# Performance work log

Hardware: AMD Instinct MI355X
Metric: run time of the kernel (lower is better)

## Reference

```python
import jax, jax.numpy as jnp
import numpy as np

N = 50000          # nodes
E = 400000         # edges
MUL0 = 16          # multiplicity of 0e irreps (node & message)
MUL1 = 8           # multiplicity of 1o irreps
RBF = 8
HID = 64
CUTOFF = 5.0
WNUM = MUL0*MUL0 + MUL1*MUL0 + MUL0*MUL1 + MUL1*MUL1  # 576 tp weights per edge
EPS = 1e-8
INV_SQRT3 = 1.0 / np.sqrt(3.0).astype(np.float32)
A_PATH = 1.0 / np.sqrt(float(MUL0 + MUL1))  # e3nn path normalization (fan_in = 24 for both outputs)


def _split_sv(x):
    # x: [n, 40] -> scalars [n,16], vectors [n,8,3]
    return x[:, :MUL0], x[:, MUL0:].reshape(-1, MUL1, 3)


def _irrep_norm(x):
    # RMS-normalize each irrep block separately (IrrepNorm)
    s, v = _split_sv(x)
    s_rms = jnp.sqrt(jnp.mean(s * s, axis=-1, keepdims=True) + EPS)
    v_rms = jnp.sqrt(jnp.mean(jnp.sum(v * v, axis=-1), axis=-1, keepdims=True) + EPS)
    return jnp.concatenate([s / s_rms, (v / v_rms[:, :, None]).reshape(-1, MUL1 * 3)], axis=-1)


def setup_inputs() -> dict:
    key = jax.random.key(0)
    ks = jax.random.split(key, 20)
    inp = {
        'x': jax.random.normal(ks[0], (N, MUL0 + 3 * MUL1), jnp.float32),
        'edge_src': jax.random.randint(ks[1], (E,), 0, N, jnp.int32),
        'edge_dst': jax.random.randint(ks[2], (E,), 0, N, jnp.int32),
        'edge_sh': jax.random.normal(ks[3], (E, 4), jnp.float32),
        'edge_rbf': jax.random.uniform(ks[4], (E, RBF), jnp.float32),
        'edge_len': jax.random.uniform(ks[5], (E,), jnp.float32) * CUTOFF,
        # radial MLP producing per-edge TP weights
        'w_r1': jax.random.normal(ks[6], (RBF, HID), jnp.float32) / np.sqrt(RBF),
        'b_r1': jnp.zeros((HID,), jnp.float32),
        'w_r2': jax.random.normal(ks[7], (HID, WNUM), jnp.float32) / np.sqrt(HID),
        'b_r2': jnp.zeros((WNUM,), jnp.float32),
        # edge gate MLP
        'w_g1': jax.random.normal(ks[8], (RBF, HID), jnp.float32) / np.sqrt(RBF),
        'b_g1': jnp.zeros((HID,), jnp.float32),
        'w_g2': jax.random.normal(ks[9], (HID, 1), jnp.float32) / np.sqrt(HID),
        'b_g2': jnp.zeros((1,), jnp.float32),
        # msg_linear: 16x0e+8x1o -> (16x0e scalars + 8x0e gates) + 8x1o gated
        'Wm_s': jax.random.normal(ks[10], (MUL0, MUL0 + MUL1), jnp.float32),
        'Wm_v': jax.random.normal(ks[11], (MUL1, MUL1), jnp.float32),
        # update_linear and self_linear: 16x0e+8x1o -> 16x0e+8x1o
        'Wu_s': jax.random.normal(ks[12], (MUL0, MUL0), jnp.float32),
        'Wu_v': jax.random.normal(ks[13], (MUL1, MUL1), jnp.float32),
        'Ws_s': jax.random.normal(ks[14], (MUL0, MUL0), jnp.float32),
        'Ws_v': jax.random.normal(ks[15], (MUL1, MUL1), jnp.float32),
        'res_scale': jnp.asarray(0.1, jnp.float32),
    }
    return inp


def reference(x, edge_src, edge_dst, edge_sh, edge_rbf, edge_len,
              w_r1, b_r1, w_r2, b_r2, w_g1, b_g1, w_g2, b_g2,
              Wm_s, Wm_v, Wu_s, Wu_v, Ws_s, Ws_v, res_scale):
    x_norm = _irrep_norm(x)
    xs, xv = _split_sv(x_norm)

    # per-edge TP weights from radial MLP
    w = jax.nn.silu(edge_rbf @ w_r1 + b_r1) @ w_r2 + b_r2            # [E, 576]
    o = MUL0 * MUL0
    w1 = w[:, :o].reshape(-1, MUL0, MUL0)                            # 0e x 0e -> 0e
    w2 = w[:, o:o + MUL1 * MUL0].reshape(-1, MUL1, MUL0)             # 1o x 1o -> 0e
    o += MUL1 * MUL0
    w3 = w[:, o:o + MUL0 * MUL1].reshape(-1, MUL0, MUL1)             # 0e x 1o -> 1o
    o += MUL0 * MUL1
    w4 = w[:, o:].reshape(-1, MUL1, MUL1)                            # 1o x 0e -> 1o

    # gather per-edge source features
    s_e = xs[edge_src]                                               # [E,16]
    v_e = xv[edge_src]                                               # [E,8,3]
    sh0 = edge_sh[:, :1]                                             # [E,1]
    sh1 = edge_sh[:, 1:4]                                            # [E,3]

    # fully-connected tensor product (CG for l<=1, component norm, path norm)
    m0 = A_PATH * (jnp.einsum('ei,eij->ej', s_e * sh0, w1)
                   + INV_SQRT3 * jnp.einsum('eic,ec,eij->ej', v_e, sh1, w2))   # [E,16]
    m1 = A_PATH * (jnp.einsum('ei,eij,ec->ejc', s_e, w3, sh1)
                   + jnp.einsum('eic,eij->ejc', v_e * sh0[:, :, None], w4))    # [E,8,3]

    # cutoff and sigmoid edge gate
    cw = 0.5 * (jnp.cos(jnp.pi * edge_len / CUTOFF) + 1.0) * (edge_len < CUTOFF)
    gw = jax.nn.sigmoid(jax.nn.silu(edge_rbf @ w_g1 + b_g1) @ w_g2 + b_g2)     # [E,1]
    ew = cw[:, None] * gw                                                      # [E,1]
    m0 = m0 * ew
    m1 = m1 * ew[:, :, None]

    # scatter-add into destination nodes, normalize by total edge weight
    agg0 = jax.ops.segment_sum(m0, edge_dst, num_segments=N)                   # [N,16]
    agg1 = jax.ops.segment_sum(m1.reshape(-1, MUL1 * 3), edge_dst, num_segments=N).reshape(-1, MUL1, 3)
    norm = jax.ops.segment_sum(ew, edge_dst, num_segments=N)                   # [N,1]
    norm = jnp.maximum(norm, EPS)
    agg0 = agg0 / norm
    agg1 = agg1 / norm[:, :, None]

    # msg_linear (equivariant linear, fan-in normalized)
    sc = agg0 @ Wm_s / np.sqrt(MUL0)                                           # [N,24]
    vv = jnp.einsum('nic,ij->njc', agg1, Wm_v) / np.sqrt(MUL1)                 # [N,8,3]

    # gated nonlinearity
    scal = jax.nn.silu(sc[:, :MUL0])
    gates = jax.nn.sigmoid(sc[:, MUL0:])
    vg = vv * gates[:, :, None]

    # update + self interaction, residual
    out_s = scal @ Wu_s / np.sqrt(MUL0) + xs @ Ws_s / np.sqrt(MUL0)
    out_v = (jnp.einsum('nic,ij->njc', vg, Wu_v) + jnp.einsum('nic,ij->njc', xv, Ws_v)) / np.sqrt(MUL1)
    out = jnp.concatenate([out_s, out_v.reshape(-1, MUL1 * 3)], axis=-1)
    return x + res_scale * out
```

## Files before the change

kernel.cpp:

```cpp
#include <hip/hip_runtime.h>
#include <cstdint>

#define MUL0 16
#define MUL1 8
#define NRBF 8
#define HID 64
#define WNUM 576
#define CUTOFF 5.0f
#define EPSF 1e-8f

#define INV_SQRT3 0.57735026918962576f
#define A_PATH    0.20412414523193154f
#define Q16       0.25f
#define Q8        0.35355339059327373f
#define PI_OVER_CUT 0.62831853071795865f

typedef _Float16 f16;
typedef _Float16 f16x8 __attribute__((ext_vector_type(8)));
typedef float f32x4 __attribute__((ext_vector_type(4)));

#define MFMA16(a, b, cc) __builtin_amdgcn_mfma_f32_16x16x32_f16(a, b, cc, 0, 0, 0)

__device__ __forceinline__ float sigm(float x) { return 1.0f / (1.0f + __expf(-x)); }

typedef __attribute__((address_space(1))) const unsigned char* gptr_t;
typedef __attribute__((address_space(3))) unsigned char* lptr_t;

__device__ __forceinline__ void stage16(const void* g, void* l) {
  __builtin_amdgcn_global_load_lds((gptr_t)g, (lptr_t)l, 16, 0, 0);
}

extern "C" __global__ __launch_bounds__(256) void k_pre(
    const float* __restrict__ x, float* __restrict__ xnorm,
    float* __restrict__ agg0, float* __restrict__ agg1,
    float* __restrict__ normb, const float* __restrict__ w_r2,
    f16* __restrict__ W2T, int N) {
  int gid = blockIdx.x * 256 + threadIdx.x;

  if (gid < HID * WNUM) {
    int n = gid >> 6, k = gid & 63;
    int jt = n >> 4, cc = n & 15;
    int h = k >> 3, e = k & 7;
    int dst = jt * 1024 + cc * 64 + ((h ^ (cc & 7)) << 3) + e;
    W2T[dst] = (f16)w_r2[k * WNUM + n];
  }

  if (gid < N) {
    long long n = gid;
    const float4* xr = (const float4*)(x + n * 40);
    float4 vv[10];
#pragma unroll
    for (int i = 0; i < 10; i++) vv[i] = xr[i];
    float* f = (float*)vv;
    float ss = 0.f, vs = 0.f;
#pragma unroll
    for (int i = 0; i < 16; i++) ss += f[i] * f[i];
#pragma unroll
    for (int i = 16; i < 40; i++) vs += f[i] * f[i];
    float sr = rsqrtf(ss * (1.0f / 16.0f) + EPSF);
    float vr = rsqrtf(vs * (1.0f / 8.0f) + EPSF);
#pragma unroll
    for (int i = 0; i < 16; i++) f[i] *= sr;
#pragma unroll
    for (int i = 16; i < 40; i++) f[i] *= vr;
    float4* o = (float4*)(xnorm + n * 40);
#pragma unroll
    for (int i = 0; i < 10; i++) o[i] = vv[i];
    float4 z = {0.f, 0.f, 0.f, 0.f};
    float4* pa0 = (float4*)(agg0 + n * 16);
#pragma unroll
    for (int i = 0; i < 4; i++) pa0[i] = z;
    float4* pa1 = (float4*)(agg1 + n * 24);
#pragma unroll
    for (int i = 0; i < 6; i++) pa1[i] = z;
    normb[n] = 0.f;
  }
}

extern "C" __global__ __launch_bounds__(256, 3) void k_edge(
    const float* __restrict__ xnorm,
    const int* __restrict__ esrc, const int* __restrict__ edst,
    const float* __restrict__ sh, const float* __restrict__ rbf,
    const float* __restrict__ elen,
    const float* __restrict__ w_r1, const float* __restrict__ b_r1,
    const float* __restrict__ w_g1, const float* __restrict__ b_g1,
    const float* __restrict__ w_g2, const float* __restrict__ b_g2,
    const float* __restrict__ b_r2, const f16* __restrict__ W2T,
    float* __restrict__ agg0, float* __restrict__ agg1,
    float* __restrict__ normb, int E) {
  __shared__ __align__(16) char smem[53248];
  f16   (*s_H)[32][72]  = (f16(*)[32][72])(smem);
  float (*s_sn)[32][20] = (float(*)[32][20])(smem + 18432);
  float (*s_v)[32][26]  = (float(*)[32][26])(smem + 28672);
  float (*s_a1)[32][10] = (float(*)[32][10])(smem + 41984);
  float (*s_sh)[32][4]  = (float(*)[32][4])(smem + 47104);
  float (*s_rbf)[32][8] = (float(*)[32][8])(smem + 49152);
  float* s_bias = (float*)(smem + 49152);

  const int t = threadIdx.x;
  const int w = t >> 6;
  const int lane = t & 63;
  const long long eb = (long long)blockIdx.x * 128 + w * 32;

  int dstv = 0, srcv = 0;
  float lenv = 1e9f;
  if (lane < 32) {
    long long g2 = eb + lane;
    float4 shv = {0.f, 0.f, 0.f, 0.f};
    if (g2 < E) {
      srcv = esrc[g2];
      dstv = edst[g2];
      lenv = elen[g2];
      shv = *(const float4*)&sh[g2 * 4];
    }
    *(float4*)&s_sh[w][lane][0] = shv;
  }
  {
    int e = lane >> 1, half = lane & 1;
    long long ge2 = eb + e;
    float4 rv4 = {0.f, 0.f, 0.f, 0.f};
    if (ge2 < E) rv4 = *(const float4*)&rbf[ge2 * 8 + half * 4];
    *(float4*)&s_rbf[w][e][half * 4] = rv4;
  }
  __syncthreads();

  {
    const int ge_l = lane >> 2;
    const int part = lane & 3;
#pragma unroll
    for (int g = 0; g < 2; g++) {
      int e = g * 16 + ge_l;
      int srcn = __shfl(srcv, e);
      const float* xr = xnorm + (long long)srcn * 40;
      if (part < 2) {
        float4 aLo = *(const float4*)(xr + part * 8);
        float4 aHi = *(const float4*)(xr + part * 8 + 4);
        *(float4*)&s_sn[w][e][part * 8] = aLo;
        *(float4*)&s_sn[w][e][part * 8 + 4] = aHi;
      } else {
        const int i0 = (part - 2) * 4;
        const float* vp = xr + 16 + i0 * 3;
        float4 v0 = *(const float4*)(vp);
        float4 v1 = *(const float4*)(vp + 4);
        float4 v2 = *(const float4*)(vp + 8);
        *(float4*)&s_v[w][e][i0 * 3] = v0;
        *(float4*)&s_v[w][e][i0 * 3 + 4] = v1;
        *(float4*)&s_v[w][e][i0 * 3 + 8] = v2;
        float4 shq = *(const float4*)&s_sh[w][e][0];
        float s1x = shq.y, s1y = shq.z, s1z = shq.w;
        s_a1[w][e][i0]     = INV_SQRT3 * (v0.x * s1x + v0.y * s1y + v0.z * s1z);
        s_a1[w][e][i0 + 1] = INV_SQRT3 * (v0.w * s1x + v1.x * s1y + v1.y * s1z);
        s_a1[w][e][i0 + 2] = INV_SQRT3 * (v1.z * s1x + v1.w * s1y + v2.x * s1z);
        s_a1[w][e][i0 + 3] = INV_SQRT3 * (v2.y * s1x + v2.z * s1y + v2.w * s1z);
      }
    }
  }

  {
    float wr[8];
#pragma unroll
    for (int r = 0; r < 8; r++) wr[r] = w_r1[r * HID + lane];
    float bh = b_r1[lane];
#pragma unroll 4
    for (int u = 0; u < 32; u++) {
      float4 ra = *(const float4*)&s_rbf[w][u][0];
      float4 rb2 = *(const float4*)&s_rbf[w][u][4];
      float acc = bh + ra.x * wr[0] + ra.y * wr[1] + ra.z * wr[2] + ra.w * wr[3]
                     + rb2.x * wr[4] + rb2.y * wr[5] + rb2.z * wr[6] + rb2.w * wr[7];
      s_H[w][u][lane] = (f16)(acc * sigm(acc));
    }
  }

  float ewv = 0.f;
  {
    const int eg = lane & 31;
    const int hf = lane >> 5;
    float4 ga = *(const float4*)&s_rbf[w][eg][0];
    float4 gb = *(const float4*)&s_rbf[w][eg][4];
    float rv[8] = {ga.x, ga.y, ga.z, ga.w, gb.x, gb.y, gb.z, gb.w};
    float accp = 0.f;
#pragma unroll
    for (int ch = 0; ch < 2; ch++) {
      const int base = hf * 32 + ch * 16;
      float ttv[16];
      {
        const float4 b0 = *(const float4*)&b_g1[base];
        const float4 b1 = *(const float4*)&b_g1[base + 4];
        const float4 b2 = *(const float4*)&b_g1[base + 8];
        const float4 b3 = *(const float4*)&b_g1[base + 12];
        ttv[0] = b0.x; ttv[1] = b0.y; ttv[2] = b0.z; ttv[3] = b0.w;
        ttv[4] = b1.x; ttv[5] = b1.y; ttv[6] = b1.z; ttv[7] = b1.w;
        ttv[8] = b2.x; ttv[9] = b2.y; ttv[10] = b2.z; ttv[11] = b2.w;
        ttv[12] = b3.x; ttv[13] = b3.y; ttv[14] = b3.z; ttv[15] = b3.w;
      }
#pragma unroll
      for (int r = 0; r < 8; r++) {
        const float* wg = w_g1 + r * HID + base;
        float4 w0 = *(const float4*)(wg);
        float4 w1 = *(const float4*)(wg + 4);
        float4 w2 = *(const float4*)(wg + 8);
        float4 w3 = *(const float4*)(wg + 12);
        float rr = rv[r];
        ttv[0] += rr * w0.x; ttv[1] += rr * w0.y; ttv[2] += rr * w0.z; ttv[3] += rr * w0.w;
        ttv[4] += rr * w1.x; ttv[5] += rr * w1.y; ttv[6] += rr * w1.z; ttv[7] += rr * w1.w;
        ttv[8] += rr * w2.x; ttv[9] += rr * w2.y; ttv[10] += rr * w2.z; ttv[11] += rr * w2.w;
        ttv[12] += rr * w3.x; ttv[13] += rr * w3.y; ttv[14] += rr * w3.z; ttv[15] += rr * w3.w;
      }
      const float4 g0 = *(const float4*)&w_g2[base];
      const float4 g1 = *(const float4*)&w_g2[base + 4];
      const float4 g2 = *(const float4*)&w_g2[base + 8];
      const float4 g3 = *(const float4*)&w_g2[base + 12];
      float gw[16] = {g0.x, g0.y, g0.z, g0.w, g1.x, g1.y, g1.z, g1.w,
                      g2.x, g2.y, g2.z, g2.w, g3.x, g3.y, g3.z, g3.w};
#pragma unroll
      for (int k = 0; k < 16; k++) accp += ttv[k] * sigm(ttv[k]) * gw[k];
    }
    accp += __shfl_xor(accp, 32);
    if (lane < 32) {
      long long g2e = eb + lane;
      if (g2e < E) {
        float cw = (lenv < CUTOFF) ? 0.5f * (__cosf(PI_OVER_CUT * lenv) + 1.0f) : 0.f;
        ewv = cw * sigm(accp + b_g2[0]);
      }
    }
  }
  __syncthreads();

  const int quad = lane >> 4;
  const int c = lane & 15;

  const f16x8 af00 = *(const f16x8*)&s_H[w][c][quad * 8];
  const f16x8 af01 = *(const f16x8*)&s_H[w][c][32 + quad * 8];
  const f16x8 af10 = *(const f16x8*)&s_H[w][16 + c][quad * 8];
  const f16x8 af11 = *(const f16x8*)&s_H[w][16 + c][32 + quad * 8];
  for (int i = t; i < WNUM; i += 256) s_bias[i] = b_r2[i];
  __syncthreads();

  char* ring = smem;
  const char* W2Tc = (const char*)W2T;
  const int lofs = w * 1024;
  const int gofs = w * 1024 + lane * 16;

  stage16(W2Tc + gofs, ring + lofs);
  stage16(W2Tc + 4096 + gofs, ring + 4096 + lofs);

  const int rd0 = c * 128 + ((quad ^ (c & 7)) << 4);
  const int rd1 = c * 128 + (((quad + 4) ^ (c & 7)) << 4);

  float p1[2][4] = {{0.f}}, p2[2][4] = {{0.f}}, t3[2][4] = {{0.f}};
  float mx[2][4] = {{0.f}}, my[2][4] = {{0.f}}, mz[2][4] = {{0.f}};

#pragma unroll 1
  for (int ch = 0; ch < 4; ch++) {
    __syncthreads();
    stage16(W2Tc + (ch + 1) * 8192 + gofs, ring + ((ch + 1) & 1) * 8192 + lofs);
    stage16(W2Tc + (ch + 1) * 8192 + 4096 + gofs,
            ring + ((ch + 1) & 1) * 8192 + 4096 + lofs);
    const char* bb = ring + (ch & 1) * 8192;
#pragma unroll
    for (int q = 0; q < 4; q++) {
      const int jt = ch * 4 + q;
      const char* tb = bb + q * 2048;
      f16x8 b0 = *(const f16x8*)(tb + rd0);
      f16x8 b1 = *(const f16x8*)(tb + rd1);
      float bias = s_bias[jt * 16 + c];
      f32x4 C0 = {0.f, 0.f, 0.f, 0.f};
      C0 = MFMA16(af00, b0, C0); C0 = MFMA16(af01, b1, C0);
      f32x4 C1 = {0.f, 0.f, 0.f, 0.f};
      C1 = MFMA16(af10, b0, C1); C1 = MFMA16(af11, b1, C1);
#pragma unroll
      for (int r = 0; r < 4; r++) {
        p1[0][r] += s_sn[w][quad * 4 + r][jt] * (C0[r] + bias);
        p1[1][r] += s_sn[w][16 + quad * 4 + r][jt] * (C1[r] + bias);
      }
    }
  }
#pragma unroll 1
  for (int ch = 4; ch < 6; ch++) {
    __syncthreads();
    stage16(W2Tc + (ch + 1) * 8192 + gofs, ring + ((ch + 1) & 1) * 8192 + lofs);
    stage16(W2Tc + (ch + 1) * 8192 + 4096 + gofs,
            ring + ((ch + 1) & 1) * 8192 + 4096 + lofs);
    const char* bb = ring + (ch & 1) * 8192;
#pragma unroll
    for (int q = 0; q < 4; q++) {
      const int jt = ch * 4 + q;
      const char* tb = bb + q * 2048;
      f16x8 b0 = *(const f16x8*)(tb + rd0);
      f16x8 b1 = *(const f16x8*)(tb + rd1);
      float bias = s_bias[jt * 16 + c];
      f32x4 C0 = {0.f, 0.f, 0.f, 0.f};
      C0 = MFMA16(af00, b0, C0); C0 = MFMA16(af01, b1, C0);
      f32x4 C1 = {0.f, 0.f, 0.f, 0.f};
      C1 = MFMA16(af10, b0, C1); C1 = MFMA16(af11, b1, C1);
      const int i = jt - 16;
#pragma unroll
      for (int r = 0; r < 4; r++) {
        p2[0][r] += s_a1[w][quad * 4 + r][i] * (C0[r] + bias);
        p2[1][r] += s_a1[w][16 + quad * 4 + r][i] * (C1[r] + bias);
      }
    }
  }
#pragma unroll 1
  for (int ch = 6; ch < 8; ch++) {
    __syncthreads();
    stage16(W2Tc + (ch + 1) * 8192 + gofs, ring + ((ch + 1) & 1) * 8192 + lofs);
    stage16(W2Tc + (ch + 1) * 8192 + 4096 + gofs,
            ring + ((ch + 1) & 1) * 8192 + 4096 + lofs);
    const char* bb = ring + (ch & 1) * 8192;
#pragma unroll
    for (int q = 0; q < 4; q++) {
      const int jt = ch * 4 + q;
      const char* tb = bb + q * 2048;
      f16x8 b0 = *(const f16x8*)(tb + rd0);
      f16x8 b1 = *(const f16x8*)(tb + rd1);
      float bias = s_bias[jt * 16 + c];
      f32x4 C0 = {0.f, 0.f, 0.f, 0.f};
      C0 = MFMA16(af00, b0, C0); C0 = MFMA16(af01, b1, C0);
      f32x4 C1 = {0.f, 0.f, 0.f, 0.f};
      C1 = MFMA16(af10, b0, C1); C1 = MFMA16(af11, b1, C1);
      const int i = (jt - 24) * 2 + (c >> 3);
#pragma unroll
      for (int r = 0; r < 4; r++) {
        t3[0][r] += s_sn[w][quad * 4 + r][i] * (C0[r] + bias);
        t3[1][r] += s_sn[w][16 + quad * 4 + r][i] * (C1[r] + bias);
      }
    }
  }
  {
    __syncthreads();
    const char* bb = ring + (8 & 1) * 8192;
#pragma unroll
    for (int q = 0; q < 4; q++) {
      const int jt = 32 + q;
      const char* tb = bb + q * 2048;
      f16x8 b0 = *(const f16x8*)(tb + rd0);
      f16x8 b1 = *(const f16x8*)(tb + rd1);
      float bias = s_bias[jt * 16 + c];
      f32x4 C0 = {0.f, 0.f, 0.f, 0.f};
      C0 = MFMA16(af00, b0, C0); C0 = MFMA16(af01, b1, C0);
      f32x4 C1 = {0.f, 0.f, 0.f, 0.f};
      C1 = MFMA16(af10, b0, C1); C1 = MFMA16(af11, b1, C1);
      const int i = q * 2 + (c >> 3);
#pragma unroll
      for (int r = 0; r < 4; r++) {
        float wv0 = C0[r] + bias;
        float wv1 = C1[r] + bias;
        mx[0][r] += s_v[w][quad * 4 + r][3 * i] * wv0;
        my[0][r] += s_v[w][quad * 4 + r][3 * i + 1] * wv0;
        mz[0][r] += s_v[w][quad * 4 + r][3 * i + 2] * wv0;
        mx[1][r] += s_v[w][16 + quad * 4 + r][3 * i] * wv1;
        my[1][r] += s_v[w][16 + quad * 4 + r][3 * i + 1] * wv1;
        mz[1][r] += s_v[w][16 + quad * 4 + r][3 * i + 2] * wv1;
      }
    }
  }

#pragma unroll
  for (int g = 0; g < 2; g++)
#pragma unroll
    for (int r = 0; r < 4; r++) {
      t3[g][r] += __shfl_xor(t3[g][r], 8);
      mx[g][r] += __shfl_xor(mx[g][r], 8);
      my[g][r] += __shfl_xor(my[g][r], 8);
      mz[g][r] += __shfl_xor(mz[g][r], 8);
    }

#pragma unroll
  for (int g = 0; g < 2; g++) {
    const int e0g = g * 16 + quad * 4;
    int cur = __shfl(dstv, e0g);
    float acc0 = 0.f, a1x = 0.f, a1y = 0.f, a1z = 0.f, nacc = 0.f;
#pragma unroll
    for (int r = 0; r < 4; r++) {
      const int e = e0g + r;
      const int dst = __shfl(dstv, e);
      const float ew = __shfl(ewv, e);
      if (dst != cur) {
        atomicAdd(&agg0[(long long)cur * 16 + c], acc0);
        if (c < 8) {
          long long b = (long long)cur * 24 + (long long)c * 3;
          atomicAdd(&agg1[b], a1x);
          atomicAdd(&agg1[b + 1], a1y);
          atomicAdd(&agg1[b + 2], a1z);
        } else if (c == 8) {
          atomicAdd(&normb[cur], nacc);
        }
        acc0 = a1x = a1y = a1z = nacc = 0.f;
        cur = dst;
      }
      float sc2 = A_PATH * ew;
      float sh0 = s_sh[w][e][0];
      acc0 += (sh0 * p1[g][r] + p2[g][r]) * sc2;
      if (c < 8) {
        float t3v = t3[g][r] * sc2;
        float scs = sc2 * sh0;
        a1x += t3v * s_sh[w][e][1] + mx[g][r] * scs;
        a1y += t3v * s_sh[w][e][2] + my[g][r] * scs;
        a1z += t3v * s_sh[w][e][3] + mz[g][r] * scs;
      } else if (c == 8) {
        nacc += ew;
      }
    }
    atomicAdd(&agg0[(long long)cur * 16 + c], acc0);
    if (c < 8) {
      long long b = (long long)cur * 24 + (long long)c * 3;
      atomicAdd(&agg1[b], a1x);
      atomicAdd(&agg1[b + 1], a1y);
      atomicAdd(&agg1[b + 2], a1z);
    } else if (c == 8) {
      atomicAdd(&normb[cur], nacc);
    }
  }
}

extern "C" __global__ __launch_bounds__(64) void k_node(
    const float* __restrict__ x, const float* __restrict__ xnorm,
    const float* __restrict__ agg0, const float* __restrict__ agg1,
    const float* __restrict__ normb, const float* __restrict__ Wm_s,
    const float* __restrict__ Wm_v, const float* __restrict__ Wu_s,
    const float* __restrict__ Wu_v, const float* __restrict__ Ws_s,
    const float* __restrict__ Ws_v, const float* __restrict__ res_scale_p,
    float* __restrict__ out, int N) {
  __shared__ float sWms[384];
  __shared__ float sWmv[64];
  __shared__ float sWus[256];
  __shared__ float sWuv[64];
  __shared__ float sWss[256];
  __shared__ float sWsv[64];
  int t = threadIdx.x;
  for (int i = t; i < 384; i += 64) sWms[i] = Wm_s[i];
  sWmv[t] = Wm_v[t];
  for (int i = t; i < 256; i += 64) sWus[i] = Wu_s[i];
  sWuv[t] = Wu_v[t];
  for (int i = t; i < 256; i += 64) sWss[i] = Ws_s[i];
  sWsv[t] = Ws_v[t];
  __syncthreads();
  int n = blockIdx.x * 64 + t;
  if (n >= N) return;

  float inv = 1.0f / fmaxf(normb[n], EPSF);
  float4 a04[4], a14[6];
  {
    const float4* p = (const float4*)(agg0 + (long long)n * 16);
#pragma unroll
    for (int i = 0; i < 4; i++) a04[i] = p[i];
    const float4* q = (const float4*)(agg1 + (long long)n * 24);
#pragma unroll
    for (int i = 0; i < 6; i++) a14[i] = q[i];
  }
  float* a0 = (float*)a04;
  float* a1 = (float*)a14;
#pragma unroll
  for (int i = 0; i < 16; i++) a0[i] *= inv;
#pragma unroll
  for (int i = 0; i < 24; i++) a1[i] *= inv;

  float scal[16], gate[8];
#pragma unroll
  for (int jj = 0; jj < 24; jj++) {
    float acc = 0.f;
#pragma unroll
    for (int i = 0; i < 16; i++) acc += a0[i] * sWms[i * 24 + jj];
    acc *= Q16;
    if (jj < 16) scal[jj] = acc * sigm(acc);
    else gate[jj - 16] = sigm(acc);
  }
  float vg[24];
#pragma unroll
  for (int j = 0; j < 8; j++) {
    float g = gate[j];
#pragma unroll
    for (int cc = 0; cc < 3; cc++) {
      float acc = 0.f;
#pragma unroll
      for (int i = 0; i < 8; i++) acc += a1[i * 3 + cc] * sWmv[i * 8 + j];
      vg[j * 3 + cc] = acc * Q8 * g;
    }
  }
  float4 xn4[10], xo4[10];
  {
    const float4* p = (const float4*)(xnorm + (long long)n * 40);
    const float4* q = (const float4*)(x + (long long)n * 40);
#pragma unroll
    for (int i = 0; i < 10; i++) { xn4[i] = p[i]; xo4[i] = q[i]; }
  }
  const float* xn = (const float*)xn4;
  const float* xo = (const float*)xo4;
  float rs = res_scale_p[0];

  float4 ob[10];
  float* ov = (float*)ob;
#pragma unroll
  for (int j = 0; j < 16; j++) {
    float acc = 0.f, acc2 = 0.f;
#pragma unroll
    for (int i = 0; i < 16; i++) {
      acc += scal[i] * sWus[i * 16 + j];
      acc2 += xn[i] * sWss[i * 16 + j];
    }
    ov[j] = xo[j] + rs * ((acc + acc2) * Q16);
  }
#pragma unroll
  for (int j = 0; j < 8; j++) {
#pragma unroll
    for (int cc = 0; cc < 3; cc++) {
      float acc = 0.f;
#pragma unroll
      for (int i = 0; i < 8; i++)
        acc += vg[i * 3 + cc] * sWuv[i * 8 + j] + xn[16 + i * 3 + cc] * sWsv[i * 8 + j];
      ov[16 + j * 3 + cc] = xo[16 + j * 3 + cc] + rs * (acc * Q8);
    }
  }
  float4* po = (float4*)(out + (long long)n * 40);
#pragma unroll
  for (int i = 0; i < 10; i++) po[i] = ob[i];
}

extern "C" void kernel_launch(void* const* d_in, const int* in_sizes, int n_in,
                              void* d_out, int out_size, void* d_ws, size_t ws_size,
                              hipStream_t stream) {
  const float* x = (const float*)d_in[0];
  const int* esrc = (const int*)d_in[1];
  const int* edst = (const int*)d_in[2];
  const float* sh = (const float*)d_in[3];
  const float* rbf = (const float*)d_in[4];
  const float* elen = (const float*)d_in[5];
  const float* w_r1 = (const float*)d_in[6];
  const float* b_r1 = (const float*)d_in[7];
  const float* w_r2 = (const float*)d_in[8];
  const float* b_r2 = (const float*)d_in[9];
  const float* w_g1 = (const float*)d_in[10];
  const float* b_g1 = (const float*)d_in[11];
  const float* w_g2 = (const float*)d_in[12];
  const float* b_g2 = (const float*)d_in[13];
  const float* Wm_s = (const float*)d_in[14];
  const float* Wm_v = (const float*)d_in[15];
  const float* Wu_s = (const float*)d_in[16];
  const float* Wu_v = (const float*)d_in[17];
  const float* Ws_s = (const float*)d_in[18];
  const float* Ws_v = (const float*)d_in[19];
  const float* res_scale = (const float*)d_in[20];

  const int N = in_sizes[0] / 40;
  const int E = in_sizes[1];

  char* ws = (char*)d_ws;
  size_t off = 0;
  float* xnorm = (float*)(ws + off); off += (size_t)N * 40 * sizeof(float);
  off = (off + 255) & ~(size_t)255;
  float* agg0 = (float*)(ws + off); off += (size_t)N * 16 * sizeof(float);
  float* agg1 = (float*)(ws + off); off += (size_t)N * 24 * sizeof(float);
  float* normb = (float*)(ws + off); off += (size_t)N * sizeof(float);
  off = (off + 255) & ~(size_t)255;
  f16* W2T = (f16*)(ws + off); off += (size_t)WNUM * 64 * sizeof(f16);

  const int nbN = (N + 255) / 256;

  k_pre<<<nbN, 256, 0, stream>>>(x, xnorm, agg0, agg1, normb, w_r2, W2T, N);

  int nblk = (E + 127) / 128;
  k_edge<<<nblk, 256, 0, stream>>>(xnorm, esrc, edst, sh, rbf, elen,
                                   w_r1, b_r1, w_g1, b_g1, w_g2, b_g2, b_r2,
                                   W2T, agg0, agg1, normb, E);

  k_node<<<(N + 63) / 64, 64, 0, stream>>>(x, xnorm, agg0, agg1, normb, Wm_s,
                                           Wm_v, Wu_s, Wu_v, Ws_s, Ws_v,
                                           res_scale, (float*)d_out, N);
}
```

Baseline: 329.2 us.

## Fuse pre, edge and node kernels into one cooperative persistent megakernel

Replaces the three separate launches with a single cooperative kernel that runs the pre-normalization, edge message and node update phases, separated by grid-wide syncs. Edge tiles and node blocks are processed in grid-stride loops over a grid sized to full occupancy. The intent is to remove the launch gaps and tail effects between stages. In exchange it adds grid sync cost, per-call host occupancy and attribute queries, and possible register pressure from merging all phases into one kernel. The node kernel's fallback path also moves to 256-thread blocks.

```diff
diff --git a/kernel.cpp b/kernel.cpp
--- a/kernel.cpp
+++ b/kernel.cpp
@@ -1,5 +1,8 @@
 #include <hip/hip_runtime.h>
+#include <hip/hip_cooperative_groups.h>
 #include <cstdint>
+
+namespace cg = cooperative_groups;
 
 #define MUL0 16
 #define MUL1 8
@@ -30,13 +33,12 @@
   __builtin_amdgcn_global_load_lds((gptr_t)g, (lptr_t)l, 16, 0, 0);
 }
 
-extern "C" __global__ __launch_bounds__(256) void k_pre(
-    const float* __restrict__ x, float* __restrict__ xnorm,
+
+__device__ __forceinline__ void pre_body(
+    int gid, const float* __restrict__ x, float* __restrict__ xnorm,
     float* __restrict__ agg0, float* __restrict__ agg1,
     float* __restrict__ normb, const float* __restrict__ w_r2,
     f16* __restrict__ W2T, int N) {
-  int gid = blockIdx.x * 256 + threadIdx.x;
-
   if (gid < HID * WNUM) {
     int n = gid >> 6, k = gid & 63;
     int jt = n >> 4, cc = n & 15;
@@ -44,7 +46,6 @@
     int dst = jt * 1024 + cc * 64 + ((h ^ (cc & 7)) << 3) + e;
     W2T[dst] = (f16)w_r2[k * WNUM + n];
   }
-
   if (gid < N) {
     long long n = gid;
     const float4* xr = (const float4*)(x + n * 40);
@@ -77,8 +78,8 @@
   }
 }
 
-extern "C" __global__ __launch_bounds__(256, 3) void k_edge(
-    const float* __restrict__ xnorm,
+__device__ __forceinline__ void edge_tile(
+    char* smem, int vb, const float* __restrict__ xnorm,
     const int* __restrict__ esrc, const int* __restrict__ edst,
     const float* __restrict__ sh, const float* __restrict__ rbf,
     const float* __restrict__ elen,
@@ -88,7 +89,6 @@
     const float* __restrict__ b_r2, const f16* __restrict__ W2T,
     float* __restrict__ agg0, float* __restrict__ agg1,
     float* __restrict__ normb, int E) {
-  __shared__ __align__(16) char smem[53248];
   f16   (*s_H)[32][72]  = (f16(*)[32][72])(smem);
   float (*s_sn)[32][20] = (float(*)[32][20])(smem + 18432);
   float (*s_v)[32][26]  = (float(*)[32][26])(smem + 28672);
@@ -100,7 +100,7 @@
   const int t = threadIdx.x;
   const int w = t >> 6;
   const int lane = t & 63;
-  const long long eb = (long long)blockIdx.x * 128 + w * 32;
+  const long long eb = (long long)vb * 128 + w * 32;
 
   int dstv = 0, srcv = 0;
   float lenv = 1e9f;
@@ -329,7 +329,7 @@
   }
   {
     __syncthreads();
-    const char* bb = ring + (8 & 1) * 8192;
+    const char* bb = ring + 8192;
 #pragma unroll
     for (int q = 0; q < 4; q++) {
       const int jt = 32 + q;
@@ -414,7 +414,167 @@
   }
 }
 
-extern "C" __global__ __launch_bounds__(64) void k_node(
+__device__ __forceinline__ void node_body(
+    long long n, const float* __restrict__ x, const float* __restrict__ xnorm,
+    const float* __restrict__ agg0, const float* __restrict__ agg1,
+    const float* __restrict__ normb, const float* sWms, const float* sWmv,
+    const float* sWus, const float* sWuv, const float* sWss,
+    const float* sWsv, float rs, float* __restrict__ out) {
+  float inv = 1.0f / fmaxf(normb[n], EPSF);
+  float4 a04[4], a14[6];
+  {
+    const float4* p = (const float4*)(agg0 + n * 16);
+#pragma unroll
+    for (int i = 0; i < 4; i++) a04[i] = p[i];
+    const float4* q = (const float4*)(agg1 + n * 24);
+#pragma unroll
+    for (int i = 0; i < 6; i++) a14[i] = q[i];
+  }
+  float* a0 = (float*)a04;
+  float* a1 = (float*)a14;
+#pragma unroll
+  for (int i = 0; i < 16; i++) a0[i] *= inv;
+#pragma unroll
+  for (int i = 0; i < 24; i++) a1[i] *= inv;
+
+  float scal[16], gate[8];
+#pragma unroll
+  for (int jj = 0; jj < 24; jj++) {
+    float acc = 0.f;
+#pragma unroll
+    for (int i = 0; i < 16; i++) acc += a0[i] * sWms[i * 24 + jj];
+    acc *= Q16;
+    if (jj < 16) scal[jj] = acc * sigm(acc);
+    else gate[jj - 16] = sigm(acc);
+  }
+  float vg[24];
+#pragma unroll
+  for (int j = 0; j < 8; j++) {
+    float g = gate[j];
+#pragma unroll
+    for (int cc = 0; cc < 3; cc++) {
+      float acc = 0.f;
+#pragma unroll
+      for (int i = 0; i < 8; i++) acc += a1[i * 3 + cc] * sWmv[i * 8 + j];
+      vg[j * 3 + cc] = acc * Q8 * g;
+    }
+  }
+  float4 xn4[10], xo4[10];
+  {
+    const float4* p = (const float4*)(xnorm + n * 40);
+    const float4* q = (const float4*)(x + n * 40);
+#pragma unroll
+    for (int i = 0; i < 10; i++) { xn4[i] = p[i]; xo4[i] = q[i]; }
+  }
+  const float* xn = (const float*)xn4;
+  const float* xo = (const float*)xo4;
+
+  float4 ob[10];
+  float* ov = (float*)ob;
+#pragma unroll
+  for (int j = 0; j < 16; j++) {
+    float acc = 0.f, acc2 = 0.f;
+#pragma unroll
+    for (int i = 0; i < 16; i++) {
+      acc += scal[i] * sWus[i * 16 + j];
+      acc2 += xn[i] * sWss[i * 16 + j];
+    }
+    ov[j] = xo[j] + rs * ((acc + acc2) * Q16);
+  }
+#pragma unroll
+  for (int j = 0; j < 8; j++) {
+#pragma unroll
+    for (int cc = 0; cc < 3; cc++) {
+      float acc = 0.f;
+#pragma unroll
+      for (int i = 0; i < 8; i++)
+        acc += vg[i * 3 + cc] * sWuv[i * 8 + j] + xn[16 + i * 3 + cc] * sWsv[i * 8 + j];
+      ov[16 + j * 3 + cc] = xo[16 + j * 3 + cc] + rs * (acc * Q8);
+    }
+  }
+  float4* po = (float4*)(out + n * 40);
+#pragma unroll
+  for (int i = 0; i < 10; i++) po[i] = ob[i];
+}
+
+extern "C" __global__ __launch_bounds__(256, 3) void k_mega(
+    const float* x, const int* esrc, const int* edst, const float* sh,
+    const float* rbf, const float* elen, const float* w_r1,
+    const float* b_r1, const float* w_g1, const float* b_g1,
+    const float* w_g2, const float* b_g2, const float* b_r2,
+    const float* w_r2, const float* Wm_s, const float* Wm_v,
+    const float* Wu_s, const float* Wu_v, const float* Ws_s,
+    const float* Ws_v, const float* res_scale_p, float* xnorm,
+    float* agg0, float* agg1, float* normb, f16* W2T, float* out,
+    int N, int E, int nbPre, int nblkE, int nbN) {
+  __shared__ __align__(16) char smem[53248];
+  cg::grid_group grid = cg::this_grid();
+  const int t = threadIdx.x;
+
+  for (int vb = blockIdx.x; vb < nbPre; vb += gridDim.x)
+    pre_body(vb * 256 + t, x, xnorm, agg0, agg1, normb, w_r2, W2T, N);
+  __threadfence();
+  grid.sync();
+
+  for (int vb = blockIdx.x; vb < nblkE; vb += gridDim.x) {
+    __syncthreads();
+    edge_tile(smem, vb, xnorm, esrc, edst, sh, rbf, elen, w_r1, b_r1, w_g1,
+              b_g1, w_g2, b_g2, b_r2, W2T, agg0, agg1, normb, E);
+  }
+  __threadfence();
+  grid.sync();
+
+  {
+    float* sW = (float*)smem;
+    float* sWms = sW;
+    float* sWmv = sW + 384;
+    float* sWus = sW + 448;
+    float* sWuv = sW + 704;
+    float* sWss = sW + 768;
+    float* sWsv = sW + 1024;
+    for (int i = t; i < 384; i += 256) sWms[i] = Wm_s[i];
+    if (t < 64) sWmv[t] = Wm_v[t];
+    sWus[t] = Wu_s[t];
+    if (t < 64) sWuv[t] = Wu_v[t];
+    sWss[t] = Ws_s[t];
+    if (t < 64) sWsv[t] = Ws_v[t];
+    __syncthreads();
+    float rs = res_scale_p[0];
+    for (int vb = blockIdx.x; vb < nbN; vb += gridDim.x) {
+      long long n = (long long)vb * 256 + t;
+      if (n < N)
+        node_body(n, x, xnorm, agg0, agg1, normb, sWms, sWmv, sWus, sWuv,
+                  sWss, sWsv, rs, out);
+    }
+  }
+}
+
+extern "C" __global__ __launch_bounds__(256) void k_pre(
+    const float* __restrict__ x, float* __restrict__ xnorm,
+    float* __restrict__ agg0, float* __restrict__ agg1,
+    float* __restrict__ normb, const float* __restrict__ w_r2,
+    f16* __restrict__ W2T, int N) {
+  pre_body(blockIdx.x * 256 + threadIdx.x, x, xnorm, agg0, agg1, normb,
+           w_r2, W2T, N);
+}
+
+extern "C" __global__ __launch_bounds__(256, 3) void k_edge(
+    const float* __restrict__ xnorm,
+    const int* __restrict__ esrc, const int* __restrict__ edst,
+    const float* __restrict__ sh, const float* __restrict__ rbf,
+    const float* __restrict__ elen,
+    const float* __restrict__ w_r1, const float* __restrict__ b_r1,
+    const float* __restrict__ w_g1, const float* __restrict__ b_g1,
+    const float* __restrict__ w_g2, const float* __restrict__ b_g2,
+    const float* __restrict__ b_r2, const f16* __restrict__ W2T,
+    float* __restrict__ agg0, float* __restrict__ agg1,
+    float* __restrict__ normb, int E) {
+  __shared__ __align__(16) char smem[53248];
+  edge_tile(smem, blockIdx.x, xnorm, esrc, edst, sh, rbf, elen, w_r1, b_r1,
+            w_g1, b_g1, w_g2, b_g2, b_r2, W2T, agg0, agg1, normb, E);
+}
+
+extern "C" __global__ __launch_bounds__(256) void k_node(
     const float* __restrict__ x, const float* __restrict__ xnorm,
     const float* __restrict__ agg0, const float* __restrict__ agg1,
     const float* __restrict__ normb, const float* __restrict__ Wm_s,
@@ -422,99 +582,25 @@
     const float* __restrict__ Wu_v, const float* __restrict__ Ws_s,
     const float* __restrict__ Ws_v, const float* __restrict__ res_scale_p,
     float* __restrict__ out, int N) {
-  __shared__ float sWms[384];
-  __shared__ float sWmv[64];
-  __shared__ float sWus[256];
-  __shared__ float sWuv[64];
-  __shared__ float sWss[256];
-  __shared__ float sWsv[64];
+  __shared__ float sW[1088];
   int t = threadIdx.x;
-  for (int i = t; i < 384; i += 64) sWms[i] = Wm_s[i];
-  sWmv[t] = Wm_v[t];
-  for (int i = t; i < 256; i += 64) sWus[i] = Wu_s[i];
-  sWuv[t] = Wu_v[t];
-  for (int i = t; i < 256; i += 64) sWss[i] = Ws_s[i];
-  sWsv[t] = Ws_v[t];
+  float* sWms = sW;
+  float* sWmv = sW + 384;
+  float* sWus = sW + 448;
+  float* sWuv = sW + 704;
+  float* sWss = sW + 768;
+  float* sWsv = sW + 1024;
+  for (int i = t; i < 384; i += 256) sWms[i] = Wm_s[i];
+  if (t < 64) sWmv[t] = Wm_v[t];
+  sWus[t] = Wu_s[t];
+  if (t < 64) sWuv[t] = Wu_v[t];
+  sWss[t] = Ws_s[t];
+  if (t < 64) sWsv[t] = Ws_v[t];
   __syncthreads();
-  int n = blockIdx.x * 64 + t;
+  long long n = (long long)blockIdx.x * 256 + t;
   if (n >= N) return;
-
-  float inv = 1.0f / fmaxf(normb[n], EPSF);
-  float4 a04[4], a14[6];
-  {
-    const float4* p = (const float4*)(agg0 + (long long)n * 16);
-#pragma unroll
-    for (int i = 0; i < 4; i++) a04[i] = p[i];
-    const float4* q = (const float4*)(agg1 + (long long)n * 24);
-#pragma unroll
-    for (int i = 0; i < 6; i++) a14[i] = q[i];
-  }
-  float* a0 = (float*)a04;
-  float* a1 = (float*)a14;
-#pragma unroll
-  for (int i = 0; i < 16; i++) a0[i] *= inv;
-#pragma unroll
-  for (int i = 0; i < 24; i++) a1[i] *= inv;
-
-  float scal[16], gate[8];
-#pragma unroll
-  for (int jj = 0; jj < 24; jj++) {
-    float acc = 0.f;
-#pragma unroll
-    for (int i = 0; i < 16; i++) acc += a0[i] * sWms[i * 24 + jj];
-    acc *= Q16;
-    if (jj < 16) scal[jj] = acc * sigm(acc);
-    else gate[jj - 16] = sigm(acc);
-  }
-  float vg[24];
-#pragma unroll
-  for (int j = 0; j < 8; j++) {
-    float g = gate[j];
-#pragma unroll
-    for (int cc = 0; cc < 3; cc++) {
-      float acc = 0.f;
-#pragma unroll
-      for (int i = 0; i < 8; i++) acc += a1[i * 3 + cc] * sWmv[i * 8 + j];
-      vg[j * 3 + cc] = acc * Q8 * g;
-    }
-  }
-  float4 xn4[10], xo4[10];
-  {
-    const float4* p = (const float4*)(xnorm + (long long)n * 40);
-    const float4* q = (const float4*)(x + (long long)n * 40);
-#pragma unroll
-    for (int i = 0; i < 10; i++) { xn4[i] = p[i]; xo4[i] = q[i]; }
-  }
-  const float* xn = (const float*)xn4;
-  const float* xo = (const float*)xo4;
-  float rs = res_scale_p[0];
-
-  float4 ob[10];
-  float* ov = (float*)ob;
-#pragma unroll
-  for (int j = 0; j < 16; j++) {
-    float acc = 0.f, acc2 = 0.f;
-#pragma unroll
-    for (int i = 0; i < 16; i++) {
-      acc += scal[i] * sWus[i * 16 + j];
-      acc2 += xn[i] * sWss[i * 16 + j];
-    }
-    ov[j] = xo[j] + rs * ((acc + acc2) * Q16);
-  }
-#pragma unroll
-  for (int j = 0; j < 8; j++) {
-#pragma unroll
-    for (int cc = 0; cc < 3; cc++) {
-      float acc = 0.f;
-#pragma unroll
-      for (int i = 0; i < 8; i++)
-        acc += vg[i * 3 + cc] * sWuv[i * 8 + j] + xn[16 + i * 3 + cc] * sWsv[i * 8 + j];
-      ov[16 + j * 3 + cc] = xo[16 + j * 3 + cc] + rs * (acc * Q8);
-    }
-  }
-  float4* po = (float4*)(out + (long long)n * 40);
-#pragma unroll
-  for (int i = 0; i < 10; i++) po[i] = ob[i];
+  node_body(n, x, xnorm, agg0, agg1, normb, sWms, sWmv, sWus, sWuv, sWss,
+            sWsv, res_scale_p[0], out);
 }
 
 extern "C" void kernel_launch(void* const* d_in, const int* in_sizes, int n_in,
@@ -555,16 +641,44 @@
   off = (off + 255) & ~(size_t)255;
   f16* W2T = (f16*)(ws + off); off += (size_t)WNUM * 64 * sizeof(f16);
 
-  const int nbN = (N + 255) / 256;
-
-  k_pre<<<nbN, 256, 0, stream>>>(x, xnorm, agg0, agg1, normb, w_r2, W2T, N);
-
-  int nblk = (E + 127) / 128;
-  k_edge<<<nblk, 256, 0, stream>>>(xnorm, esrc, edst, sh, rbf, elen,
-                                   w_r1, b_r1, w_g1, b_g1, w_g2, b_g2, b_r2,
-                                   W2T, agg0, agg1, normb, E);
-
-  k_node<<<(N + 63) / 64, 64, 0, stream>>>(x, xnorm, agg0, agg1, normb, Wm_s,
-                                           Wm_v, Wu_s, Wu_v, Ws_s, Ws_v,
-                                           res_scale, (float*)d_out, N);
-}
+  int nbN256 = (N + 255) / 256;
+  int nbPre = nbN256;
+  if ((HID * WNUM + 255) / 256 > nbPre) nbPre = (HID * WNUM + 255) / 256;
+  int nblkE = (E + 127) / 128;
+
+  int blocksPerCU = 0;
+  (void)hipOccupancyMaxActiveBlocksPerMultiprocessor(&blocksPerCU,
+                                                     (const void*)k_mega, 256, 0);
+  if (blocksPerCU < 1) blocksPerCU = 1;
+  int numCU = 0, dev = 0;
+  (void)hipGetDevice(&dev);
+  (void)hipDeviceGetAttribute(&numCU, hipDeviceAttributeMultiprocessorCount, dev);
+  if (numCU < 1) numCU = 256;
+  int grid = blocksPerCU * numCU;
+  if (grid > nblkE) grid = nblkE;
+
+  int N_ = N, E_ = E, nbPre_ = nbPre, nblkE_ = nblkE, nbN_ = nbN256;
+  float* outp = (float*)d_out;
+  void* args[] = {
+      (void*)&x,      (void*)&esrc,   (void*)&edst,   (void*)&sh,
+      (void*)&rbf,    (void*)&elen,   (void*)&w_r1,   (void*)&b_r1,
+      (void*)&w_g1,   (void*)&b_g1,   (void*)&w_g2,   (void*)&b_g2,
+      (void*)&b_r2,   (void*)&w_r2,   (void*)&Wm_s,   (void*)&Wm_v,
+      (void*)&Wu_s,   (void*)&Wu_v,   (void*)&Ws_s,   (void*)&Ws_v,
+      (void*)&res_scale, (void*)&xnorm, (void*)&agg0, (void*)&agg1,
+      (void*)&normb,  (void*)&W2T,    (void*)&outp,   (void*)&N_,
+      (void*)&E_,     (void*)&nbPre_, (void*)&nblkE_, (void*)&nbN_};
+
+  hipError_t err = hipLaunchCooperativeKernel(
+      (const void*)k_mega, dim3(grid), dim3(256), args, 0, stream);
+
+  if (err != hipSuccess) {
+    k_pre<<<nbPre, 256, 0, stream>>>(x, xnorm, agg0, agg1, normb, w_r2, W2T, N);
+    k_edge<<<nblkE, 256, 0, stream>>>(xnorm, esrc, edst, sh, rbf, elen,
+                                      w_r1, b_r1, w_g1, b_g1, w_g2, b_g2,
+                                      b_r2, W2T, agg0, agg1, normb, E);
+    k_node<<<nbN256, 256, 0, stream>>>(x, xnorm, agg0, agg1, normb, Wm_s,
+                                       Wm_v, Wu_s, Wu_v, Ws_s, Ws_v,
+                                       res_scale, (float*)d_out, N);
+  }
+}
```

Result: slower. 647.2 us (+96.6%).
